# Performance work log

Measured on AMD Instinct MI355X. Metric: run time of the kernel, lower is better.

The kernel has to match this reference:

```python
import jax, jax.numpy as jnp
import numpy as np

B, D, K = 16384, 32, 128  # batch, cluster_dim, num_clusters


def setup_inputs() -> dict:
    key = jax.random.key(0)
    x = jax.random.normal(key, (B, D, K), dtype=jnp.float32)
    mu_0 = jnp.zeros((D, K), dtype=jnp.float32)                      # running mean buffer
    L_0 = jnp.broadcast_to(jnp.eye(D, dtype=jnp.float32), (K, D, D)) # running Cholesky buffer
    n_0 = jnp.ones((1,), dtype=jnp.float32)                          # running count
    return {"x": x, "mu_0": mu_0, "L_0": L_0, "n_0": n_0}


def reference(x, mu_0, L_0, n_0):
    # Training-mode forward of ClusterNorm1dv2.
    Bn = x.shape[0]
    eps_eye = jnp.eye(x.shape[1], dtype=x.dtype)
    n0 = n_0[0]
    x_mu = jnp.mean(x, axis=0)                         # [D, K]
    x_cnt = jnp.transpose(x - x_mu[None], (2, 1, 0))   # [K, D, B]
    C = jnp.einsum('kdb,keb->kde', x_cnt, x_cnt)       # [K, D, D] per-cluster scatter
    denom = n0 + Bn
    new_mu = (n0 * mu_0 + Bn * x_mu) / denom           # [D, K]
    x_d = jnp.transpose((x_mu - mu_0)[None], (2, 1, 0))  # [K, D, 1]
    new_cov = (jnp.einsum('kde,kfe->kdf', L_0, L_0) * (n0 / denom)
               + C / denom
               + jnp.einsum('kdo,keo->kde', x_d, x_d) * (n0 * Bn / denom ** 2))
    L = jnp.linalg.cholesky(new_cov + eps_eye)         # [K, D, D]
    xc = jnp.transpose(x - new_mu[None], (2, 1, 0))    # [K, D, B]
    Z = jax.scipy.linalg.solve_triangular(L, xc, lower=True)  # whitening solve
    return jnp.transpose(Z, (2, 1, 0))                 # [B, D, K]
```

## Files before the change

### kernel.cpp

```cpp
#include <hip/hip_runtime.h>

typedef __attribute__((ext_vector_type(4))) float f32x4;

#define NB 16384
#define ND 32
#define NK 128

template<int SP>
__device__ __forceinline__ void k1_body(const float* __restrict__ x,
                                        float* __restrict__ part,
                                        int k0, int b0, int kl) {
  constexpr int CL = 4*(SP+1);
  constexpr int CH = 4*(8-SP);
  constexpr int NV = CH;

  float aL[4][CL];
  float aH[4][CH];
  float ssum[8];
  #pragma unroll
  for (int r=0;r<4;r++){
    #pragma unroll
    for (int c=0;c<CL;c++) aL[r][c]=0.f;
    #pragma unroll
    for (int c=0;c<CH;c++) aH[r][c]=0.f;
  }
  #pragma unroll
  for (int i=0;i<8;i++) ssum[i]=0.f;

  const float* xp = x + (size_t)b0*4096 + k0 + kl;

  for (int s=0; s<64; ++s) {
    const float* xs = xp + (size_t)s*4096;
    float v[NV];
    #pragma unroll
    for (int d=0; d<NV; ++d) v[d] = xs[d*128];
    #pragma unroll
    for (int r=0;r<4;r++){ ssum[r] += v[4*SP+r]; ssum[4+r] += v[CH-4+r]; }
    #pragma unroll
    for (int r=0;r<4;r++){
      const float al = v[4*SP+r];
      #pragma unroll
      for (int c=0;c<CL;c++) aL[r][c] += al*v[c];
      const float ah = v[CH-4+r];
      #pragma unroll
      for (int c=0;c<CH;c++) aH[r][c] += ah*v[c];
    }
  }

  float* pb = part + (size_t)blockIdx.x*38912;
  #pragma unroll
  for (int r=0;r<4;r++){
    #pragma unroll
    for (int c=0;c<CL;c++)
      __builtin_nontemporal_store(aL[r][c], &pb[(8*SP*(SP+1) + r*CL + c)*64 + kl]);
    #pragma unroll
    for (int c=0;c<CH;c++)
      __builtin_nontemporal_store(aH[r][c], &pb[(8*(7-SP)*(8-SP) + r*CH + c)*64 + kl]);
  }
  #pragma unroll
  for (int r=0;r<4;r++){
    __builtin_nontemporal_store(ssum[r],   &pb[(576 + 4*SP + r)*64 + kl]);
    __builtin_nontemporal_store(ssum[4+r], &pb[(576 + CH-4 + r)*64 + kl]);
  }
}

__global__ __launch_bounds__(256, 2) void k1_scatter(const float* __restrict__ x,
                                                     float* __restrict__ part) {
  const int t = threadIdx.x;
  const int ktile = blockIdx.x & 1;
  const int chunk = blockIdx.x >> 1;
  const int k0 = ktile*64, b0 = chunk*64;
  const int kl = t & 63;
  switch (t>>6) {
    case 0:  k1_body<0>(x, part, k0, b0, kl); break;
    case 1:  k1_body<1>(x, part, k0, b0, kl); break;
    case 2:  k1_body<2>(x, part, k0, b0, kl); break;
    default: k1_body<3>(x, part, k0, b0, kl); break;
  }
}

__global__ void k2a_reduce(const float* __restrict__ part, float* __restrict__ sfin) {
  const int t = threadIdx.x;
  const int bx = blockIdx.x;
  const int h = bx & 1, ktile = (bx>>1)&1, vg = bx>>2;
  const int vidx = vg*4 + (t>>6);
  const int kl = t & 63;
  const float* p = part + ((size_t)(h*128)*2 + ktile)*38912 + vidx*64 + kl;
  float a0=0.f,a1=0.f,a2=0.f,a3=0.f;
  for (int c=0;c<128;c+=4){
    a0 += __builtin_nontemporal_load(&p[(size_t)(c+0)*77824]);
    a1 += __builtin_nontemporal_load(&p[(size_t)(c+1)*77824]);
    a2 += __builtin_nontemporal_load(&p[(size_t)(c+2)*77824]);
    a3 += __builtin_nontemporal_load(&p[(size_t)(c+3)*77824]);
  }
  sfin[h*77824 + vidx*128 + ktile*64 + kl] = (a0+a1)+(a2+a3);
}

__global__ void k2b_chol(const float* __restrict__ sfin,
                         const float* __restrict__ mu0,
                         const float* __restrict__ L0,
                         const float* __restrict__ n0p,
                         float* __restrict__ lpad,
                         float* __restrict__ nmu) {
  const int k = blockIdx.x;
  const int t = threadIdx.x;
  __shared__ float L0s[32*33];
  __shared__ float Am[32*33];
  __shared__ float xdl[32];
  __shared__ float dinv[32];
  const float n0 = n0p[0];
  const float denom = n0 + (float)NB;

  for (int idx = t; idx < 1024; idx += 256)
    L0s[(idx>>5)*33 + (idx&31)] = L0[k*1024 + idx];
  if (t < 32) {
    const float S  = sfin[(576+t)*128 + k] + sfin[77824 + (576+t)*128 + k];
    const float m0 = mu0[t*128 + k];
    nmu[t*128 + k] = (n0*m0 + S) / denom;
    xdl[t] = S*(1.0f/NB) - m0;
  }
  __syncthreads();

  const float c1 = n0/denom, c2 = 1.0f/denom;
  const float c3 = n0*(float)NB/(denom*denom);
  for (int idx = t; idx < 1024; idx += 256) {
    const int d = idx>>5, e = idx&31;
    const int dd = d>=e?d:e, ee = d>=e?e:d;
    const int R = dd>>2;
    const int vi = 8*R*(R+1) + (dd&3)*4*(R+1) + ee;
    const float M  = sfin[vi*128 + k]      + sfin[77824 + vi*128 + k];
    const float Sd = sfin[(576+d)*128 + k] + sfin[77824 + (576+d)*128 + k];
    const float Se = sfin[(576+e)*128 + k] + sfin[77824 + (576+e)*128 + k];
    const float C = M - Sd*Se*(1.0f/NB);
    float g = 0.f;
    #pragma unroll 8
    for (int f=0; f<32; f++) g += L0s[d*33+f]*L0s[e*33+f];
    float a = g*c1 + C*c2 + xdl[d]*xdl[e]*c3;
    if (d==e) a += 1.0f;
    Am[d*33+e] = a;
  }
  __syncthreads();

  for (int j=0;j<32;j++){
    float acc = 0.f;
    if (t < 32 && t >= j) {
      acc = Am[t*33+j];
      for (int e=0;e<j;e++) acc -= Am[t*33+e]*Am[j*33+e];
    }
    __syncthreads();
    if (t == j) {
      const float dj = sqrtf(acc);
      Am[j*33+j] = dj;
      dinv[j] = 1.0f/dj;
    }
    __syncthreads();
    if (t < 32 && t > j) Am[t*33+j] = acc*dinv[j];
    __syncthreads();
  }

  if (t < 32) {
    const int d = t;
    int rs = 0;
    for (int e=0;e<d;e++) rs += (e+3)>>2;
    rs *= 4;
    const int rl = ((d+3)>>2)*4;
    float* lp = lpad + k*576;
    for (int e=0;e<rl;e++) lp[rs+e] = (e<d) ? Am[d*33+e] : 0.f;
    lp[544+d] = dinv[d];
  }
}

__global__ __launch_bounds__(256, 2) void k3_whiten(const float* __restrict__ x,
                                                    const float* __restrict__ lpad,
                                                    const float* __restrict__ nmu,
                                                    float* __restrict__ out) {
  __shared__ float Lw[32*580];
  __shared__ float muL[32*32];
  const int t = threadIdx.x;
  const int bx = blockIdx.x;
  const int m = (bx >> 3) & 1;
  const int u = ((bx >> 4) << 3) | (bx & 7);
  const int ktile = ((u & 1) << 1) | m;
  const int chunk = u >> 1;
  const int k0 = ktile*32;

  {
    const f32x4* src = (const f32x4*)(lpad + (size_t)k0*576);
    #pragma unroll
    for (int q=0;q<18;q++){
      const int idx = t + q*256;
      const int row = idx/144, col = idx - row*144;
      *(f32x4*)(&Lw[row*580 + col*4]) = src[idx];
    }
    #pragma unroll
    for (int idx=t; idx<1024; idx+=256)
      muL[idx] = nmu[(idx>>5)*128 + k0 + (idx&31)];
  }
  __syncthreads();

  const int kl = t & 31;
  const int so = t >> 5;
  const float* Lrow = &Lw[kl*580];
  const int b0 = chunk*128;

  for (int it=0; it<4; ++it) {
    const int base = b0 + it*32 + so;
    const float* xa = x + (size_t)(base     )*4096 + k0 + kl;
    const float* xb = x + (size_t)(base +  8)*4096 + k0 + kl;
    const float* xc = x + (size_t)(base + 16)*4096 + k0 + kl;
    const float* xd = x + (size_t)(base + 24)*4096 + k0 + kl;
    float vA[32], vB[32], vC[32], vD[32];
    #pragma unroll
    for (int d=0; d<32; ++d) vA[d] = xa[d*128];
    #pragma unroll
    for (int d=0; d<32; ++d) vB[d] = xb[d*128];
    #pragma unroll
    for (int d=0; d<32; ++d) vC[d] = xc[d*128];
    #pragma unroll
    for (int d=0; d<32; ++d) vD[d] = xd[d*128];
    #pragma unroll
    for (int d=0; d<32; ++d) {
      const float m2 = muL[d*32 + kl];
      vA[d] -= m2; vB[d] -= m2; vC[d] -= m2; vD[d] -= m2;
    }
    int rs = 0;
    #pragma unroll
    for (int d=0; d<32; ++d) {
      float sA = vA[d], sB = vB[d], sC = vC[d], sD = vD[d];
      const int nq = (d+3)>>2;
      #pragma unroll
      for (int q=0; q<nq; ++q) {
        const f32x4 Lq = *(const f32x4*)(Lrow + rs + 4*q);
        sA -= Lq[0]*vA[4*q+0] + Lq[1]*vA[4*q+1] + Lq[2]*vA[4*q+2] + Lq[3]*vA[4*q+3];
        sB -= Lq[0]*vB[4*q+0] + Lq[1]*vB[4*q+1] + Lq[2]*vB[4*q+2] + Lq[3]*vB[4*q+3];
        sC -= Lq[0]*vC[4*q+0] + Lq[1]*vC[4*q+1] + Lq[2]*vC[4*q+2] + Lq[3]*vC[4*q+3];
        sD -= Lq[0]*vD[4*q+0] + Lq[1]*vD[4*q+1] + Lq[2]*vD[4*q+2] + Lq[3]*vD[4*q+3];
      }
      const float di = Lrow[544+d];
      vA[d] = sA*di; vB[d] = sB*di; vC[d] = sC*di; vD[d] = sD*di;
      rs += 4*nq;
    }
    float* oa = out + (size_t)(base     )*4096 + k0 + kl;
    float* ob = out + (size_t)(base +  8)*4096 + k0 + kl;
    float* oc = out + (size_t)(base + 16)*4096 + k0 + kl;
    float* od = out + (size_t)(base + 24)*4096 + k0 + kl;
    #pragma unroll
    for (int d=0; d<32; ++d) __builtin_nontemporal_store(vA[d], oa + d*128);
    #pragma unroll
    for (int d=0; d<32; ++d) __builtin_nontemporal_store(vB[d], ob + d*128);
    #pragma unroll
    for (int d=0; d<32; ++d) __builtin_nontemporal_store(vC[d], oc + d*128);
    #pragma unroll
    for (int d=0; d<32; ++d) __builtin_nontemporal_store(vD[d], od + d*128);
  }
}

extern "C" void kernel_launch(void* const* d_in, const int* in_sizes, int n_in,
                              void* d_out, int out_size, void* d_ws, size_t ws_size,
                              hipStream_t stream) {
  const float* x   = (const float*)d_in[0];
  const float* mu0 = (const float*)d_in[1];
  const float* L0  = (const float*)d_in[2];
  const float* n0  = (const float*)d_in[3];
  float* out  = (float*)d_out;
  float* part = out;
  float* sfin = out + 20971520;
  float* lpad = (float*)d_ws;
  float* nmu  = lpad + 128*576;

  k1_scatter<<<512, 256, 0, stream>>>(x, part);
  k2a_reduce<<<608, 256, 0, stream>>>(part, sfin);
  k2b_chol  <<<128, 256, 0, stream>>>(sfin, mu0, L0, n0, lpad, nmu);
  k3_whiten <<<512, 256, 0, stream>>>(x, lpad, nmu, out);
}
```

Measured before the change: 200.5 us.

## Compute per-cluster scatter matrices with bf16 MFMA instead of scalar FMAs

The scatter kernel now stages x tiles into shared memory as packed bf16 and computes the per-cluster 32x32 Gram matrices and column sums with 16x16x32 bf16 MFMA instructions, replacing the fp32 scalar outer-product accumulation. Partial results are laid out per cluster as full 32x32 plus sums, which simplifies the reduction and Cholesky indexing and reduces the partial count. The aim is to cut the FMA-bound cost of the covariance computation. The trade-off is that bf16 rounding of the inputs lowers covariance accuracy, and the sums computed through MFMA also see bf16-rounded values.

```diff
diff --git a/kernel.cpp b/kernel.cpp
--- a/kernel.cpp
+++ b/kernel.cpp
@@ -1,99 +1,119 @@
 #include <hip/hip_runtime.h>
 
 typedef __attribute__((ext_vector_type(4))) float f32x4;
+typedef __attribute__((ext_vector_type(8))) short short8;
 
 #define NB 16384
 #define ND 32
 #define NK 128
 
-template<int SP>
-__device__ __forceinline__ void k1_body(const float* __restrict__ x,
-                                        float* __restrict__ part,
-                                        int k0, int b0, int kl) {
-  constexpr int CL = 4*(SP+1);
-  constexpr int CH = 4*(8-SP);
-  constexpr int NV = CH;
-
-  float aL[4][CL];
-  float aH[4][CH];
-  float ssum[8];
-  #pragma unroll
-  for (int r=0;r<4;r++){
-    #pragma unroll
-    for (int c=0;c<CL;c++) aL[r][c]=0.f;
-    #pragma unroll
-    for (int c=0;c<CH;c++) aH[r][c]=0.f;
-  }
-  #pragma unroll
-  for (int i=0;i<8;i++) ssum[i]=0.f;
-
-  const float* xp = x + (size_t)b0*4096 + k0 + kl;
-
-  for (int s=0; s<64; ++s) {
-    const float* xs = xp + (size_t)s*4096;
-    float v[NV];
-    #pragma unroll
-    for (int d=0; d<NV; ++d) v[d] = xs[d*128];
-    #pragma unroll
-    for (int r=0;r<4;r++){ ssum[r] += v[4*SP+r]; ssum[4+r] += v[CH-4+r]; }
-    #pragma unroll
-    for (int r=0;r<4;r++){
-      const float al = v[4*SP+r];
-      #pragma unroll
-      for (int c=0;c<CL;c++) aL[r][c] += al*v[c];
-      const float ah = v[CH-4+r];
-      #pragma unroll
-      for (int c=0;c<CH;c++) aH[r][c] += ah*v[c];
-    }
-  }
-
-  float* pb = part + (size_t)blockIdx.x*38912;
-  #pragma unroll
-  for (int r=0;r<4;r++){
-    #pragma unroll
-    for (int c=0;c<CL;c++)
-      __builtin_nontemporal_store(aL[r][c], &pb[(8*SP*(SP+1) + r*CL + c)*64 + kl]);
-    #pragma unroll
-    for (int c=0;c<CH;c++)
-      __builtin_nontemporal_store(aH[r][c], &pb[(8*(7-SP)*(8-SP) + r*CH + c)*64 + kl]);
-  }
-  #pragma unroll
-  for (int r=0;r<4;r++){
-    __builtin_nontemporal_store(ssum[r],   &pb[(576 + 4*SP + r)*64 + kl]);
-    __builtin_nontemporal_store(ssum[4+r], &pb[(576 + CH-4 + r)*64 + kl]);
-  }
-}
-
-__global__ __launch_bounds__(256, 2) void k1_scatter(const float* __restrict__ x,
+__device__ __forceinline__ unsigned bfbits(float f){
+  union { float f; unsigned u; } v; v.f = f;
+  const unsigned u = v.u;
+  return (u + 0x7FFFu + ((u>>16)&1u)) >> 16;
+}
+__device__ __forceinline__ unsigned pkbf(float lo, float hi){
+  return bfbits(lo) | (bfbits(hi) << 16);
+}
+
+__global__ __launch_bounds__(512, 2) void k1_scatter(const float* __restrict__ x,
                                                      float* __restrict__ part) {
-  const int t = threadIdx.x;
-  const int ktile = blockIdx.x & 1;
-  const int chunk = blockIdx.x >> 1;
-  const int k0 = ktile*64, b0 = chunk*64;
-  const int kl = t & 63;
-  switch (t>>6) {
-    case 0:  k1_body<0>(x, part, k0, b0, kl); break;
-    case 1:  k1_body<1>(x, part, k0, b0, kl); break;
-    case 2:  k1_body<2>(x, part, k0, b0, kl); break;
-    default: k1_body<3>(x, part, k0, b0, kl); break;
-  }
-}
-
-__global__ void k2a_reduce(const float* __restrict__ part, float* __restrict__ sfin) {
+  __shared__ float vs[16384];
   const int t = threadIdx.x;
   const int bx = blockIdx.x;
-  const int h = bx & 1, ktile = (bx>>1)&1, vg = bx>>2;
-  const int vidx = vg*4 + (t>>6);
-  const int kl = t & 63;
-  const float* p = part + ((size_t)(h*128)*2 + ktile)*38912 + vidx*64 + kl;
+  const int ktile = bx & 3;
+  const int cb = bx >> 2;
+  const int k0 = ktile*32;
+
+  const int shalf = t >> 8;
+  const int d     = (t >> 3) & 31;
+  const int kq    = t & 7;
+  const float* xb = x + (size_t)d*128 + k0 + 4*kq;
+
+  const int l = t & 63;
+  const int w = t >> 6;
+
+  f32x4 acc[4][4];
+  f32x4 accS[4][2];
+  #pragma unroll
+  for (int c=0;c<4;c++){
+    #pragma unroll
+    for (int q=0;q<4;q++){ acc[c][q][0]=0.f; acc[c][q][1]=0.f; acc[c][q][2]=0.f; acc[c][q][3]=0.f; }
+    #pragma unroll
+    for (int q=0;q<2;q++){ accS[c][q][0]=0.f; accS[c][q][1]=0.f; accS[c][q][2]=0.f; accS[c][q][3]=0.f; }
+  }
+
+  const short8 ones = {0x3F80,0x3F80,0x3F80,0x3F80,0x3F80,0x3F80,0x3F80,0x3F80};
+  unsigned* vsw = (unsigned*)vs;
+
+  for (int ch = 0; ch < 8; ++ch) {
+    const int sb = cb*256 + ch*32 + shalf*16;
+    f32x4 La[8], Lb[8];
+    #pragma unroll
+    for (int p = 0; p < 8; ++p) {
+      const int pr = (p + kq) & 7;
+      const float* src = xb + (size_t)(sb + 2*pr)*4096;
+      La[p] = *(const f32x4*)src;
+      Lb[p] = *(const f32x4*)(src + 4096);
+    }
+    #pragma unroll
+    for (int p = 0; p < 8; ++p) {
+      const int pr = (p + kq) & 7;
+      const int sp = shalf*8 + pr;
+      #pragma unroll
+      for (int i = 0; i < 4; ++i)
+        vsw[(4*kq + i)*512 + d*16 + sp] = pkbf(La[p][i], Lb[p][i]);
+    }
+    __syncthreads();
+    #pragma unroll
+    for (int c = 0; c < 4; ++c) {
+      const int kk = w*4 + c;
+      const float* base = vs + kk*512;
+      const short8 f0 = *(const short8*)(base + (l&15)*16      + (l>>4)*4);
+      const short8 f1 = *(const short8*)(base + (l&15)*16 + 256 + (l>>4)*4);
+      acc[c][0]  = __builtin_amdgcn_mfma_f32_16x16x32_bf16(f0, f0, acc[c][0], 0,0,0);
+      acc[c][1]  = __builtin_amdgcn_mfma_f32_16x16x32_bf16(f0, f1, acc[c][1], 0,0,0);
+      acc[c][2]  = __builtin_amdgcn_mfma_f32_16x16x32_bf16(f1, f0, acc[c][2], 0,0,0);
+      acc[c][3]  = __builtin_amdgcn_mfma_f32_16x16x32_bf16(f1, f1, acc[c][3], 0,0,0);
+      accS[c][0] = __builtin_amdgcn_mfma_f32_16x16x32_bf16(f0, ones, accS[c][0], 0,0,0);
+      accS[c][1] = __builtin_amdgcn_mfma_f32_16x16x32_bf16(f1, ones, accS[c][1], 0,0,0);
+    }
+    __syncthreads();
+  }
+
+  const int col = l & 15, rw = (l >> 4) * 4;
+  #pragma unroll
+  for (int c = 0; c < 4; ++c) {
+    const int kg = k0 + w*4 + c;
+    float* pb = part + ((size_t)cb*128 + kg)*1056;
+    #pragma unroll
+    for (int i = 0; i < 2; ++i)
+      #pragma unroll
+      for (int j = 0; j < 2; ++j)
+        #pragma unroll
+        for (int r = 0; r < 4; ++r)
+          pb[(i*16 + rw + r)*32 + j*16 + col] = acc[c][i*2+j][r];
+    if (col == 0) {
+      #pragma unroll
+      for (int i = 0; i < 2; ++i)
+        #pragma unroll
+        for (int r = 0; r < 4; ++r)
+          pb[1024 + i*16 + rw + r] = accS[c][i][r];
+    }
+  }
+}
+
+__global__ void k2a_reduce(const float* __restrict__ part, float* __restrict__ sfin) {
+  const size_t idx = (size_t)blockIdx.x*256 + threadIdx.x;
+  const float* p = part + idx;
   float a0=0.f,a1=0.f,a2=0.f,a3=0.f;
-  for (int c=0;c<128;c+=4){
-    a0 += __builtin_nontemporal_load(&p[(size_t)(c+0)*77824]);
-    a1 += __builtin_nontemporal_load(&p[(size_t)(c+1)*77824]);
-    a2 += __builtin_nontemporal_load(&p[(size_t)(c+2)*77824]);
-    a3 += __builtin_nontemporal_load(&p[(size_t)(c+3)*77824]);
-  }
-  sfin[h*77824 + vidx*128 + ktile*64 + kl] = (a0+a1)+(a2+a3);
+  for (int c = 0; c < 64; c += 4) {
+    a0 += p[(size_t)(c+0)*135168];
+    a1 += p[(size_t)(c+1)*135168];
+    a2 += p[(size_t)(c+2)*135168];
+    a3 += p[(size_t)(c+3)*135168];
+  }
+  sfin[idx] = (a0+a1)+(a2+a3);
 }
 
 __global__ void k2b_chol(const float* __restrict__ sfin,
@@ -110,11 +130,12 @@
   __shared__ float dinv[32];
   const float n0 = n0p[0];
   const float denom = n0 + (float)NB;
+  const float* sk = sfin + (size_t)k*1056;
 
   for (int idx = t; idx < 1024; idx += 256)
     L0s[(idx>>5)*33 + (idx&31)] = L0[k*1024 + idx];
   if (t < 32) {
-    const float S  = sfin[(576+t)*128 + k] + sfin[77824 + (576+t)*128 + k];
+    const float S  = sk[1024 + t];
     const float m0 = mu0[t*128 + k];
     nmu[t*128 + k] = (n0*m0 + S) / denom;
     xdl[t] = S*(1.0f/NB) - m0;
@@ -125,12 +146,9 @@
   const float c3 = n0*(float)NB/(denom*denom);
   for (int idx = t; idx < 1024; idx += 256) {
     const int d = idx>>5, e = idx&31;
-    const int dd = d>=e?d:e, ee = d>=e?e:d;
-    const int R = dd>>2;
-    const int vi = 8*R*(R+1) + (dd&3)*4*(R+1) + ee;
-    const float M  = sfin[vi*128 + k]      + sfin[77824 + vi*128 + k];
-    const float Sd = sfin[(576+d)*128 + k] + sfin[77824 + (576+d)*128 + k];
-    const float Se = sfin[(576+e)*128 + k] + sfin[77824 + (576+e)*128 + k];
+    const float M  = sk[d*32 + e];
+    const float Sd = sk[1024 + d];
+    const float Se = sk[1024 + e];
     const float C = M - Sd*Se*(1.0f/NB);
     float g = 0.f;
     #pragma unroll 8
@@ -264,12 +282,12 @@
   const float* n0  = (const float*)d_in[3];
   float* out  = (float*)d_out;
   float* part = out;
-  float* sfin = out + 20971520;
+  float* sfin = out + 8650752;
   float* lpad = (float*)d_ws;
   float* nmu  = lpad + 128*576;
 
-  k1_scatter<<<512, 256, 0, stream>>>(x, part);
-  k2a_reduce<<<608, 256, 0, stream>>>(part, sfin);
+  k1_scatter<<<256, 512, 0, stream>>>(x, part);
+  k2a_reduce<<<528, 256, 0, stream>>>(part, sfin);
   k2b_chol  <<<128, 256, 0, stream>>>(sfin, mu0, L0, n0, lpad, nmu);
   k3_whiten <<<512, 256, 0, stream>>>(x, lpad, nmu, out);
 }
```

New measurement: 198.7 us. Within noise of the previous version (-0.9%).
